# Performance work log

Hardware: AMD Instinct MI355X
Metric: run time of the kernel (lower is better)

The kernel has to match this reference:

```python
import jax, jax.numpy as jnp
import numpy as np

N = 16384      # number of target nodes
NS = 16384     # number of source nodes
K = 32         # neighbors per node
CS = 256       # source_channels
CT = 256       # target_channels
CO = 64        # out_channels
M = 64         # size (number of weight matrices); must equal CO for the original code to broadcast


def setup_inputs() -> dict:
    key = jax.random.key(0)
    ks = jax.random.split(key, 9)
    source = jax.random.normal(ks[0], (NS, CS), dtype=jnp.float32)
    target = jax.random.normal(ks[1], (N, CT), dtype=jnp.float32)
    neighbors = jax.random.randint(ks[2], (N, K), 0, NS)
    # size parallel Linear(CS, CO) layers, stored [in, out]
    W_lin = jax.random.normal(ks[3], (M, CS, CO), dtype=jnp.float32) / np.sqrt(CS)
    b_lin = jax.random.normal(ks[4], (M, CO), dtype=jnp.float32) * 0.01
    # source assignment Linear(CS, M)
    W_s = jax.random.normal(ks[5], (CS, M), dtype=jnp.float32) / np.sqrt(CS)
    b_s = jax.random.normal(ks[6], (M,), dtype=jnp.float32) * 0.01
    # target assignment Linear(CT, M)
    W_t = jax.random.normal(ks[7], (CT, M), dtype=jnp.float32) / np.sqrt(CT)
    b_t = jax.random.normal(ks[8], (M,), dtype=jnp.float32) * 0.01
    return {"source": source, "target": target, "neighbors": neighbors,
            "W_lin": W_lin, "b_lin": b_lin, "W_s": W_s, "b_s": b_s,
            "W_t": W_t, "b_t": b_t}


def reference(source, target, neighbors, W_lin, b_lin, W_s, b_s, W_t, b_t):
    # gather neighbor messages: [N, K, CS]
    msgs = source[neighbors]
    # assignment logits: source proj [N, K, M] + target proj broadcast [N, 1, M]
    s_logit = jnp.einsum('nkc,cm->nkm', msgs, W_s) + b_s
    t_logit = target @ W_t + b_t                      # [N, M]
    assignment = jax.nn.softmax(s_logit + t_logit[:, None, :], axis=-1)  # [N, K, M]
    # (assignment * stack_m(msgs @ W_m)).mean over m == assignment * (msgs @ mean_m W_m)
    # because assignment is independent of m (faithful to the original math).
    W_mean = W_lin.mean(axis=0)                       # [CS, CO]
    b_mean = b_lin.mean(axis=0)                       # [CO]
    proj = jnp.einsum('nkc,co->nko', msgs, W_mean) + b_mean  # [N, K, CO]
    return assignment * proj                          # [N, K, CO]  (CO == M)
```

## Files before the change

kernel.cpp:

```cpp
#include <hip/hip_runtime.h>
#include <hip/hip_fp16.h>

typedef _Float16 f16x8 __attribute__((ext_vector_type(8)));
typedef _Float16 f16x4 __attribute__((ext_vector_type(4)));
typedef float f32x4 __attribute__((ext_vector_type(4)));

__global__ void prep_weights(const float* __restrict__ W_lin, const float* __restrict__ b_lin,
                             const float* __restrict__ W_s, const float* __restrict__ W_t,
                             _Float16* __restrict__ WcT, _Float16* __restrict__ Wt16,
                             float* __restrict__ bmean) {
    int tid = blockIdx.x * 256 + threadIdx.x;
    if (tid < 16384) {
        int c = tid >> 6, o = tid & 63;
        WcT[o * 256 + c]  = (_Float16)W_s[c * 64 + o];
        Wt16[o * 256 + c] = (_Float16)W_t[c * 64 + o];
    } else {
        int t = tid - 16384;
        int c = t >> 6, o = t & 63;
        float s = 0.f;
        #pragma unroll 8
        for (int m = 0; m < 64; ++m) s += W_lin[m * 16384 + c * 64 + o];
        WcT[(64 + o) * 256 + c] = (_Float16)(s * (1.f / 64.f));
    }
    if (tid < 64) {
        float s = 0.f;
        #pragma unroll 8
        for (int m = 0; m < 64; ++m) s += b_lin[m * 64 + tid];
        bmean[tid] = s * (1.f / 64.f);
    }
}

__device__ __forceinline__ f16x8 cvt8(const float* p) {
    f32x4 x = *(const f32x4*)p;
    f32x4 y = *(const f32x4*)(p + 4);
    f16x8 h;
    h[0] = (_Float16)x[0]; h[1] = (_Float16)x[1]; h[2] = (_Float16)x[2]; h[3] = (_Float16)x[3];
    h[4] = (_Float16)y[0]; h[5] = (_Float16)y[1]; h[6] = (_Float16)y[2]; h[7] = (_Float16)y[3];
    return h;
}

__global__ __launch_bounds__(256, 2)
void gemm_prep(const float* __restrict__ source, const float* __restrict__ target,
               const _Float16* __restrict__ WcT, const _Float16* __restrict__ Wt16,
               const float* __restrict__ bmean, const float* __restrict__ b_s,
               const float* __restrict__ b_t,
               _Float16* __restrict__ Ppe, float* __restrict__ Et) {
    __shared__ _Float16 lds[32768];

    const int tid = threadIdx.x;
    const int w = tid >> 6, l = tid & 63;
    const int l15 = l & 15, lq = l >> 4;
    const int b = blockIdx.x;

    if (b < 256) {
        const int rb = b * 64;
        const float* arow = source + (size_t)(rb + w * 16 + l15) * 256;
        f16x8 af[8];
        #pragma unroll
        for (int s = 0; s < 8; ++s) af[s] = cvt8(arow + s * 32 + lq * 8);

        #pragma unroll
        for (int i = 0; i < 16; ++i) {
            int c = i * 256 + tid;
            int fi = c >> 6, lane = c & 63;
            int nt = fi >> 3, s = fi & 7;
            f16x8 v = *(const f16x8*)(WcT + (nt * 16 + (lane & 15)) * 256 + s * 32 + (lane >> 4) * 8);
            *(f16x8*)((char*)lds + c * 16) = v;
        }
        __syncthreads();

        const char* bb = (const char*)lds + l * 16;
        f32x4 acc[8] = {};
        #pragma unroll
        for (int s = 0; s < 8; ++s) {
            #pragma unroll
            for (int nt = 0; nt < 8; ++nt) {
                f16x8 bf = *(const f16x8*)(bb + nt * 8192 + s * 1024);
                acc[nt] = __builtin_amdgcn_mfma_f32_16x16x32_f16(af[s], bf, acc[nt], 0, 0, 0);
            }
        }

        float bmv[4];
        #pragma unroll
        for (int nt = 0; nt < 4; ++nt) bmv[nt] = bmean[nt * 16 + l15];
        #pragma unroll
        for (int j = 0; j < 4; ++j) {
            int row = rb + w * 16 + lq * 4 + j;
            #pragma unroll
            for (int nt = 0; nt < 4; ++nt) {
                Ppe[row * 128 + nt * 16 + l15]        = (_Float16)__expf(acc[nt][j]);
                Ppe[row * 128 + (nt + 4) * 16 + l15]  = (_Float16)(acc[nt + 4][j] + bmv[nt]);
            }
        }
    } else {
        const int rb = (b - 256) * 64;
        const float* arow = target + (size_t)(rb + w * 16 + l15) * 256;
        f16x8 af[8];
        #pragma unroll
        for (int s = 0; s < 8; ++s) af[s] = cvt8(arow + s * 32 + lq * 8);

        #pragma unroll
        for (int i = 0; i < 8; ++i) {
            int c = i * 256 + tid;
            int fi = c >> 6, lane = c & 63;
            int nt = fi >> 3, s = fi & 7;
            f16x8 v = *(const f16x8*)(Wt16 + (nt * 16 + (lane & 15)) * 256 + s * 32 + (lane >> 4) * 8);
            *(f16x8*)((char*)lds + c * 16) = v;
        }
        __syncthreads();

        const char* bb = (const char*)lds + l * 16;
        f32x4 acc[4] = {};
        #pragma unroll
        for (int s = 0; s < 8; ++s) {
            #pragma unroll
            for (int nt = 0; nt < 4; ++nt) {
                f16x8 bf = *(const f16x8*)(bb + nt * 8192 + s * 1024);
                acc[nt] = __builtin_amdgcn_mfma_f32_16x16x32_f16(af[s], bf, acc[nt], 0, 0, 0);
            }
        }

        float bsv[4];
        #pragma unroll
        for (int nt = 0; nt < 4; ++nt) {
            int col = nt * 16 + l15;
            bsv[nt] = b_s[col] + b_t[col];
        }
        #pragma unroll
        for (int j = 0; j < 4; ++j) {
            int row = rb + w * 16 + lq * 4 + j;
            #pragma unroll
            for (int nt = 0; nt < 4; ++nt)
                Et[row * 64 + nt * 16 + l15] = __expf(acc[nt][j] + bsv[nt]);
        }
    }
}

__global__ __launch_bounds__(256)
void epilogue(const int* __restrict__ neighbors, const _Float16* __restrict__ Ppe,
              const float* __restrict__ Et, float* __restrict__ out) {
    const int tid = threadIdx.x;
    const int w = tid >> 6, l = tid & 63;
    const int lq = l >> 4, l15 = l & 15;
    const int n0 = blockIdx.x * 8 + w * 2;
    const int co = l15 * 4;

    f32x4 et0 = *(const f32x4*)(Et + n0 * 64 + co);
    f32x4 et1 = *(const f32x4*)(Et + (n0 + 1) * 64 + co);

    int nb0[8], nb1[8];
    #pragma unroll
    for (int g = 0; g < 8; ++g) nb0[g] = neighbors[n0 * 32 + g * 4 + lq];
    #pragma unroll
    for (int g = 0; g < 8; ++g) nb1[g] = neighbors[(n0 + 1) * 32 + g * 4 + lq];

    f16x4 pe0[8], pp0[8], pe1[8], pp1[8];
    #pragma unroll
    for (int g = 0; g < 8; ++g) {
        pe0[g] = *(const f16x4*)(Ppe + nb0[g] * 128 + co);
        pp0[g] = *(const f16x4*)(Ppe + nb0[g] * 128 + 64 + co);
    }
    #pragma unroll
    for (int g = 0; g < 8; ++g) {
        pe1[g] = *(const f16x4*)(Ppe + nb1[g] * 128 + co);
        pp1[g] = *(const f16x4*)(Ppe + nb1[g] * 128 + 64 + co);
    }

    #pragma unroll
    for (int g = 0; g < 8; ++g) {
        float w0 = (float)pe0[g][0] * et0[0];
        float w1 = (float)pe0[g][1] * et0[1];
        float w2 = (float)pe0[g][2] * et0[2];
        float w3 = (float)pe0[g][3] * et0[3];
        float s = (w0 + w1) + (w2 + w3);
        s += __shfl_xor(s, 1);
        s += __shfl_xor(s, 2);
        s += __shfl_xor(s, 4);
        s += __shfl_xor(s, 8);
        float inv = 1.0f / s;
        f32x4 o;
        o[0] = w0 * inv * (float)pp0[g][0];
        o[1] = w1 * inv * (float)pp0[g][1];
        o[2] = w2 * inv * (float)pp0[g][2];
        o[3] = w3 * inv * (float)pp0[g][3];
        *(f32x4*)(out + (size_t)(n0 * 32 + g * 4 + lq) * 64 + co) = o;
    }
    #pragma unroll
    for (int g = 0; g < 8; ++g) {
        float w0 = (float)pe1[g][0] * et1[0];
        float w1 = (float)pe1[g][1] * et1[1];
        float w2 = (float)pe1[g][2] * et1[2];
        float w3 = (float)pe1[g][3] * et1[3];
        float s = (w0 + w1) + (w2 + w3);
        s += __shfl_xor(s, 1);
        s += __shfl_xor(s, 2);
        s += __shfl_xor(s, 4);
        s += __shfl_xor(s, 8);
        float inv = 1.0f / s;
        f32x4 o;
        o[0] = w0 * inv * (float)pp1[g][0];
        o[1] = w1 * inv * (float)pp1[g][1];
        o[2] = w2 * inv * (float)pp1[g][2];
        o[3] = w3 * inv * (float)pp1[g][3];
        *(f32x4*)(out + (size_t)((n0 + 1) * 32 + g * 4 + lq) * 64 + co) = o;
    }
}

extern "C" void kernel_launch(void* const* d_in, const int* in_sizes, int n_in,
                              void* d_out, int out_size, void* d_ws, size_t ws_size,
                              hipStream_t stream) {
    const float* source    = (const float*)d_in[0];
    const float* target    = (const float*)d_in[1];
    const int*   neighbors = (const int*)d_in[2];
    const float* W_lin     = (const float*)d_in[3];
    const float* b_lin     = (const float*)d_in[4];
    const float* W_s       = (const float*)d_in[5];
    const float* b_s       = (const float*)d_in[6];
    const float* W_t       = (const float*)d_in[7];
    const float* b_t       = (const float*)d_in[8];

    char* ws = (char*)d_ws;
    _Float16* Ppe   = (_Float16*)ws;
    float*    Et    = (float*)(ws + (4u << 20));
    _Float16* WcT   = (_Float16*)(ws + (8u << 20));
    _Float16* Wt16  = (_Float16*)(ws + (8u << 20) + 65536);
    float*    bmean = (float*)(ws + (8u << 20) + 98304);
    float*    out   = (float*)d_out;

    prep_weights<<<128, 256, 0, stream>>>(W_lin, b_lin, W_s, W_t, WcT, Wt16, bmean);
    gemm_prep<<<512, 256, 0, stream>>>(source, target, WcT, Wt16, bmean, b_s, b_t,
                                       Ppe, Et);
    epilogue<<<2048, 256, 0, stream>>>(neighbors, Ppe, Et, out);
}
```

Before: 54.13 us.

## Drop LDS staging in gemm_prep and split source GEMM columns across waves

Removes the shared-memory staging of the fp16 weight matrices and the block barrier, so each wave loads B fragments straight from global memory (L2-resident, since the weights are small). The source GEMM is split so each wave computes only 64 of the 128 output columns (the exp half or the projection half), which halves the accumulator count and doubles the grid to 768 blocks. The launch bound is raised to 4 blocks per CU. In exchange, every wave now reads the weights from global memory instead of LDS, and each source row's A fragment is loaded and converted twice.

```diff
diff --git a/kernel.cpp b/kernel.cpp
--- a/kernel.cpp
+++ b/kernel.cpp
@@ -39,83 +39,64 @@
     return h;
 }
 
-__global__ __launch_bounds__(256, 2)
+__global__ __launch_bounds__(256, 4)
 void gemm_prep(const float* __restrict__ source, const float* __restrict__ target,
                const _Float16* __restrict__ WcT, const _Float16* __restrict__ Wt16,
                const float* __restrict__ bmean, const float* __restrict__ b_s,
                const float* __restrict__ b_t,
                _Float16* __restrict__ Ppe, float* __restrict__ Et) {
-    __shared__ _Float16 lds[32768];
-
     const int tid = threadIdx.x;
     const int w = tid >> 6, l = tid & 63;
     const int l15 = l & 15, lq = l >> 4;
     const int b = blockIdx.x;
 
-    if (b < 256) {
-        const int rb = b * 64;
-        const float* arow = source + (size_t)(rb + w * 16 + l15) * 256;
+    if (b < 512) {
+        const int h  = w & 1;
+        const int rb = b * 32 + (w >> 1) * 16;
+        const float* arow = source + (size_t)(rb + l15) * 256;
         f16x8 af[8];
         #pragma unroll
         for (int s = 0; s < 8; ++s) af[s] = cvt8(arow + s * 32 + lq * 8);
 
-        #pragma unroll
-        for (int i = 0; i < 16; ++i) {
-            int c = i * 256 + tid;
-            int fi = c >> 6, lane = c & 63;
-            int nt = fi >> 3, s = fi & 7;
-            f16x8 v = *(const f16x8*)(WcT + (nt * 16 + (lane & 15)) * 256 + s * 32 + (lane >> 4) * 8);
-            *(f16x8*)((char*)lds + c * 16) = v;
-        }
-        __syncthreads();
-
-        const char* bb = (const char*)lds + l * 16;
-        f32x4 acc[8] = {};
+        const _Float16* bp = WcT + (size_t)(h * 64 + l15) * 256 + lq * 8;
+        f32x4 acc[4] = {};
         #pragma unroll
         for (int s = 0; s < 8; ++s) {
             #pragma unroll
-            for (int nt = 0; nt < 8; ++nt) {
-                f16x8 bf = *(const f16x8*)(bb + nt * 8192 + s * 1024);
+            for (int nt = 0; nt < 4; ++nt) {
+                f16x8 bf = *(const f16x8*)(bp + nt * 16 * 256 + s * 32);
                 acc[nt] = __builtin_amdgcn_mfma_f32_16x16x32_f16(af[s], bf, acc[nt], 0, 0, 0);
             }
         }
 
         float bmv[4];
         #pragma unroll
-        for (int nt = 0; nt < 4; ++nt) bmv[nt] = bmean[nt * 16 + l15];
+        for (int nt = 0; nt < 4; ++nt) bmv[nt] = h ? bmean[nt * 16 + l15] : 0.f;
+
         #pragma unroll
         for (int j = 0; j < 4; ++j) {
-            int row = rb + w * 16 + lq * 4 + j;
+            int row = rb + lq * 4 + j;
             #pragma unroll
             for (int nt = 0; nt < 4; ++nt) {
-                Ppe[row * 128 + nt * 16 + l15]        = (_Float16)__expf(acc[nt][j]);
-                Ppe[row * 128 + (nt + 4) * 16 + l15]  = (_Float16)(acc[nt + 4][j] + bmv[nt]);
+                float v = acc[nt][j];
+                _Float16 r = h ? (_Float16)(v + bmv[nt]) : (_Float16)__expf(v);
+                Ppe[row * 128 + h * 64 + nt * 16 + l15] = r;
             }
         }
     } else {
-        const int rb = (b - 256) * 64;
-        const float* arow = target + (size_t)(rb + w * 16 + l15) * 256;
+        const int rb = (b - 512) * 64 + w * 16;
+        const float* arow = target + (size_t)(rb + l15) * 256;
         f16x8 af[8];
         #pragma unroll
         for (int s = 0; s < 8; ++s) af[s] = cvt8(arow + s * 32 + lq * 8);
 
-        #pragma unroll
-        for (int i = 0; i < 8; ++i) {
-            int c = i * 256 + tid;
-            int fi = c >> 6, lane = c & 63;
-            int nt = fi >> 3, s = fi & 7;
-            f16x8 v = *(const f16x8*)(Wt16 + (nt * 16 + (lane & 15)) * 256 + s * 32 + (lane >> 4) * 8);
-            *(f16x8*)((char*)lds + c * 16) = v;
-        }
-        __syncthreads();
-
-        const char* bb = (const char*)lds + l * 16;
+        const _Float16* bp = Wt16 + (size_t)l15 * 256 + lq * 8;
         f32x4 acc[4] = {};
         #pragma unroll
         for (int s = 0; s < 8; ++s) {
             #pragma unroll
             for (int nt = 0; nt < 4; ++nt) {
-                f16x8 bf = *(const f16x8*)(bb + nt * 8192 + s * 1024);
+                f16x8 bf = *(const f16x8*)(bp + nt * 16 * 256 + s * 32);
                 acc[nt] = __builtin_amdgcn_mfma_f32_16x16x32_f16(af[s], bf, acc[nt], 0, 0, 0);
             }
         }
@@ -128,7 +109,7 @@
         }
         #pragma unroll
         for (int j = 0; j < 4; ++j) {
-            int row = rb + w * 16 + lq * 4 + j;
+            int row = rb + lq * 4 + j;
             #pragma unroll
             for (int nt = 0; nt < 4; ++nt)
                 Et[row * 64 + nt * 16 + l15] = __expf(acc[nt][j] + bsv[nt]);
@@ -228,7 +209,7 @@
     float*    out   = (float*)d_out;
 
     prep_weights<<<128, 256, 0, stream>>>(W_lin, b_lin, W_s, W_t, WcT, Wt16, bmean);
-    gemm_prep<<<512, 256, 0, stream>>>(source, target, WcT, Wt16, bmean, b_s, b_t,
+    gemm_prep<<<768, 256, 0, stream>>>(source, target, WcT, Wt16, bmean, b_s, b_t,
                                        Ppe, Et);
     epilogue<<<2048, 256, 0, stream>>>(neighbors, Ppe, Et, out);
 }
```

New measurement: 63.83 us. 1.18x slower.
